# Kernel optimization log

Hardware: AMD Instinct MI355X
Metric: run time of the kernel (lower is better)

The kernel has to match this reference:

```python
import jax, jax.numpy as jnp
import numpy as np

GENETIC_CODE = {'TTT': 'F', 'TTC': 'F', 'TTA': 'L', 'TTG': 'L', 'CTT': 'L', 'CTC': 'L', 'CTA': 'L', 'CTG': 'L', 'ATT': 'I', 'ATC': 'I', 'ATA': 'I', 'ATG': 'M', 'GTT': 'V', 'GTC': 'V', 'GTA': 'V', 'GTG': 'V', 'TCT': 'S', 'TCC': 'S', 'TCA': 'S', 'TCG': 'S', 'AGT': 'S', 'AGC': 'S', 'CCT': 'P', 'CCC': 'P', 'CCA': 'P', 'CCG': 'P', 'ACT': 'T', 'ACC': 'T', 'ACA': 'T', 'ACG': 'T', 'GCT': 'A', 'GCC': 'A', 'GCA': 'A', 'GCG': 'A', 'TAT': 'Y', 'TAC': 'Y', 'TAA': '*', 'TAG': '*', 'TGA': '*', 'CAT': 'H', 'CAC': 'H', 'CAA': 'Q', 'CAG': 'Q', 'AAT': 'N', 'AAC': 'N', 'AAA': 'K', 'AAG': 'K', 'GAT': 'D', 'GAC': 'D', 'GAA': 'E', 'GAG': 'E', 'TGT': 'C', 'TGC': 'C', 'TGG': 'W', 'CGT': 'R', 'CGC': 'R', 'CGA': 'R', 'CGG': 'R', 'AGA': 'R', 'AGG': 'R', 'GGT': 'G', 'GGC': 'G', 'GGA': 'G', 'GGG': 'G'}
NUC_TO_IDX = {'T': 0, 'C': 1, 'A': 2, 'G': 3}

def _build_syn_bias(synonymy_bias=1.0):
    idx = lambda c: NUC_TO_IDX[c[0]] * 16 + NUC_TO_IDX[c[1]] * 4 + NUC_TO_IDX[c[2]]
    groups = {}
    for codon, aa in GENETIC_CODE.items():
        groups.setdefault(aa, []).append(idx(codon))
    m = np.zeros((64, 64), dtype=np.float32)
    for codons in groups.values():
        for i in codons:
            for j in codons:
                m[i, j] = synonymy_bias
    return jnp.asarray(m)

HIDDEN, N_HEADS = 256, 4
HEAD_DIM = HIDDEN // N_HEADS
B, S = 2, 4096

def setup_inputs() -> dict:
    key = jax.random.key(0)
    ks = jax.random.split(key, 10)
    std = 1.0 / np.sqrt(HIDDEN)
    lin = lambda k: jax.random.uniform(k, (HIDDEN, HIDDEN), jnp.float32, -std, std)
    bias = lambda k: jax.random.uniform(k, (HIDDEN,), jnp.float32, -std, std)
    return {
        'x': jax.random.normal(ks[0], (B, S, HIDDEN), jnp.float32),
        'codons': jax.random.randint(ks[1], (B, S), 0, 64),
        'syn_bias': _build_syn_bias(1.0),
        'wq': lin(ks[2]), 'bq': bias(ks[3]),
        'wk': lin(ks[4]), 'bk': bias(ks[5]),
        'wv': lin(ks[6]), 'bv': bias(ks[7]),
        'wo': lin(ks[8]), 'bo': bias(ks[9]),
    }

def reference(x, codons, syn_bias, wq, bq, wk, bk, wv, bv, wo, bo):
    b, s, _ = x.shape
    split = lambda t: t.reshape(b, s, N_HEADS, HEAD_DIM).transpose(0, 2, 1, 3)  # (B,H,S,D)
    q = split(x @ wq.T + bq)
    k = split(x @ wk.T + bk)
    v = split(x @ wv.T + bv)
    scores = jnp.einsum('bhqd,bhkd->bhqk', q, k) / np.sqrt(HEAD_DIM)
    # gather pairwise synonymy bias: (B,S,S) broadcast over heads
    pair_bias = syn_bias[codons[:, :, None], codons[:, None, :]]
    scores = scores + pair_bias[:, None, :, :]
    attn = jax.nn.softmax(scores, axis=-1)
    out = jnp.einsum('bhqk,bhkd->bhqd', attn, v)
    out = out.transpose(0, 2, 1, 3).reshape(b, s, HIDDEN)
    return out @ wo.T + bo
```

## Files before the change

kernel.cpp:

```cpp
#include <hip/hip_runtime.h>
#include <hip/hip_bf16.h>

#define NH 4
#define HD 64
#define HID 256
#define SS 4096

#define QFRAG_PER_HEAD (128 * 6 * 64 * 8)
#define KFRAG_PER_HEAD (64 * 12 * 64 * 8)
#define VFRAG_PER_HEAD (64 * 8 * 64 * 8)

typedef float f4 __attribute__((ext_vector_type(4)));
typedef float f16v __attribute__((ext_vector_type(16)));
typedef short bf8 __attribute__((ext_vector_type(8)));
typedef unsigned int u4v __attribute__((ext_vector_type(4)));

static __device__ __forceinline__ float fast_exp2(float x) {
#if __has_builtin(__builtin_amdgcn_exp2f)
    return __builtin_amdgcn_exp2f(x);
#else
    float r; asm("v_exp_f32 %0, %1" : "=v"(r) : "v"(x)); return r;
#endif
}

static __device__ __forceinline__ unsigned pack2(float a, float b) {
    unsigned ua = (unsigned)__bfloat16_as_ushort(__float2bfloat16(a));
    unsigned ub = (unsigned)__bfloat16_as_ushort(__float2bfloat16(b));
    return ua | (ub << 16);
}

__global__ void setup_kernel(const float* __restrict__ syn,
                             int* __restrict__ gid, float* __restrict__ betaP)
{
    const int lane = threadIdx.x;
    int rep = 64;
    for (int j = 63; j >= 0; --j)
        if (syn[lane * 64 + j] != 0.0f) rep = j;
    if (rep == 64) rep = lane;
    unsigned long long m = __ballot(rep == lane);
    int id = (int)__popcll(m & ((2ull << rep) - 1ull)) - 1;
    if (id < 0) id = 0;
    gid[lane] = id;
    if (lane == 0) *betaP = syn[0] * 1.44269504088896f;
}

__global__ __launch_bounds__(256)
void pack_w_kernel(const float* __restrict__ wq, const float* __restrict__ wk,
                   const float* __restrict__ wv, const float* __restrict__ wo,
                   __hip_bfloat16* __restrict__ wpk)
{
    const int t = blockIdx.x * 256 + threadIdx.x;
    const int mat = t >> 13;
    const int r = t & 8191;
    const int dt = r >> 10, ks = (r >> 6) & 15, lane = r & 63;
    const float* w = (mat == 0) ? wq : (mat == 1) ? wk : (mat == 2) ? wv : wo;
    const int row = dt * 32 + (lane & 31);
    const int col = ks * 16 + (lane >> 5) * 8;
    const f4 a = *(const f4*)&w[(size_t)row * 256 + col];
    const f4 b = *(const f4*)&w[(size_t)row * 256 + col + 4];
    union { unsigned u[4]; bf8 v; } o;
    o.u[0] = pack2(a[0], a[1]); o.u[1] = pack2(a[2], a[3]);
    o.u[2] = pack2(b[0], b[1]); o.u[3] = pack2(b[2], b[3]);
    *(bf8*)&wpk[(size_t)t * 8] = o.v;
}

__global__ __launch_bounds__(256)
void qkv_mfma_kernel(const float* __restrict__ x,
                     const __hip_bfloat16* __restrict__ wpk,
                     const float* __restrict__ bq, const float* __restrict__ bk,
                     const float* __restrict__ bv,
                     const int* __restrict__ codons,
                     const int* __restrict__ gid, const float* __restrict__ betaP,
                     __hip_bfloat16* __restrict__ qfrag,
                     __hip_bfloat16* __restrict__ kfrag,
                     __hip_bfloat16* __restrict__ vfrag)
{
    const int bid = blockIdx.x;
    const int stile = bid / 6;
    const int grp = bid % 6;
    const int tid = threadIdx.x;
    const int w = tid >> 6, lane = tid & 63, hi = lane >> 5, l5 = lane & 31;

    const int bidx = stile >> 7;
    const int stl = stile & 127;
    const int hs = stl & 1, tkv = stl >> 1;

    __shared__ __hip_bfloat16 xs[32][256];

    {
        const int r0 = tid >> 5, c = tid & 31;
        #pragma unroll
        for (int it = 0; it < 4; ++it) {
            const int row = r0 + it * 8;
            const f4 a = *(const f4*)&x[(size_t)(stile * 32 + row) * HID + c * 8];
            const f4 b2 = *(const f4*)&x[(size_t)(stile * 32 + row) * HID + c * 8 + 4];
            union { unsigned u[4]; bf8 v; } o;
            o.u[0] = pack2(a[0], a[1]); o.u[1] = pack2(a[2], a[3]);
            o.u[2] = pack2(b2[0], b2[1]); o.u[3] = pack2(b2[2], b2[3]);
            *(bf8*)&xs[row][((c ^ row) & 31) * 8] = o.v;
        }
    }
    __syncthreads();

    const int t24 = grp * 4 + w;
    const int mat = t24 >> 3;
    const int dt = t24 & 7;
    const int head = dt >> 1, d32 = dt & 1;

    const __hip_bfloat16* wb = wpk + (size_t)((mat * 8 + dt) * 16) * 512 + (size_t)lane * 8;
    bf8 wf[16];
    #pragma unroll
    for (int ks = 0; ks < 16; ++ks) wf[ks] = *(const bf8*)&wb[ks * 512];

    f16v acc;
    #pragma unroll
    for (int r = 0; r < 16; ++r) acc[r] = 0.0f;

    if (mat < 2) {
        #pragma unroll
        for (int ks = 0; ks < 16; ++ks) {
            const bf8 xf = *(const bf8*)&xs[l5][(((ks * 2 + hi) ^ l5) & 31) * 8];
            acc = __builtin_amdgcn_mfma_f32_32x32x16_bf16(wf[ks], xf, acc, 0, 0, 0);
        }
    } else {
        #pragma unroll
        for (int ks = 0; ks < 16; ++ks) {
            const bf8 xf = *(const bf8*)&xs[l5][(((ks * 2 + hi) ^ l5) & 31) * 8];
            acc = __builtin_amdgcn_mfma_f32_32x32x16_bf16(xf, wf[ks], acc, 0, 0, 0);
        }
    }

    const float QSCALE = 0.18033688011112042f;
    if (mat == 0) {
        f4 b4[4];
        #pragma unroll
        for (int j = 0; j < 4; ++j)
            b4[j] = *(const f4*)&bq[head * 64 + d32 * 32 + j * 8 + 4 * hi];
        #pragma unroll
        for (int r = 0; r < 16; ++r) acc[r] = (acc[r] + b4[r >> 2][r & 3]) * QSCALE;
    } else if (mat == 1) {
        f4 b4[4];
        #pragma unroll
        for (int j = 0; j < 4; ++j)
            b4[j] = *(const f4*)&bk[head * 64 + d32 * 32 + j * 8 + 4 * hi];
        #pragma unroll
        for (int r = 0; r < 16; ++r) acc[r] += b4[r >> 2][r & 3];
    } else {
        const float bn = bv[head * 64 + d32 * 32 + l5];
        #pragma unroll
        for (int r = 0; r < 16; ++r) acc[r] += bn;
    }

    unsigned wd[8];
    #pragma unroll
    for (int i = 0; i < 8; ++i) wd[i] = pack2(acc[2 * i], acc[2 * i + 1]);
    const unsigned e0 = (unsigned)__shfl_xor((int)(hi ? wd[0] : wd[2]), 32, 64);
    const unsigned e1 = (unsigned)__shfl_xor((int)(hi ? wd[1] : wd[3]), 32, 64);
    const unsigned e2 = (unsigned)__shfl_xor((int)(hi ? wd[4] : wd[6]), 32, 64);
    const unsigned e3 = (unsigned)__shfl_xor((int)(hi ? wd[5] : wd[7]), 32, 64);
    union { unsigned u[4]; bf8 v; } fa, fb;
    if (hi == 0) {
        fa.u[0] = wd[0]; fa.u[1] = wd[1]; fa.u[2] = e0; fa.u[3] = e1;
        fb.u[0] = wd[4]; fb.u[1] = wd[5]; fb.u[2] = e2; fb.u[3] = e3;
    } else {
        fa.u[0] = e0; fa.u[1] = e1; fa.u[2] = wd[2]; fa.u[3] = wd[3];
        fb.u[0] = e2; fb.u[1] = e3; fb.u[2] = wd[6]; fb.u[3] = wd[7];
    }

    const int hd = bidx * NH + head;
    if (mat == 0) {
        __hip_bfloat16* qb = qfrag + (size_t)hd * QFRAG_PER_HEAD;
        *(bf8*)&qb[((size_t)(stl * 6 + d32 * 2 + 0) * 64 + lane) * 8] = fa.v;
        *(bf8*)&qb[((size_t)(stl * 6 + d32 * 2 + 1) * 64 + lane) * 8] = fb.v;
    } else if (mat == 1) {
        __hip_bfloat16* kb = kfrag + (size_t)hd * KFRAG_PER_HEAD;
        *(bf8*)&kb[((size_t)(tkv * 12 + d32 * 4 + hs) * 64 + lane) * 8] = fa.v;
        *(bf8*)&kb[((size_t)(tkv * 12 + d32 * 4 + 2 + hs) * 64 + lane) * 8] = fb.v;
    } else {
        __hip_bfloat16* vb = vfrag + (size_t)hd * VFRAG_PER_HEAD;
        const int ja = ((stl * 2 + 0) & 3) * 2 + d32;
        const int jb = ((stl * 2 + 1) & 3) * 2 + d32;
        *(bf8*)&vb[((size_t)(tkv * 8 + ja) * 64 + lane) * 8] = fa.v;
        *(bf8*)&vb[((size_t)(tkv * 8 + jb) * 64 + lane) * 8] = fb.v;
    }

    if (grp == 0) {
        const int hh = w;
        const int hd2 = bidx * NH + hh;
        __hip_bfloat16* qb = qfrag + (size_t)hd2 * QFRAG_PER_HEAD;
        __hip_bfloat16* kb = kfrag + (size_t)hd2 * KFRAG_PER_HEAD;
        u4v z; z[0] = 0; z[1] = 0; z[2] = 0; z[3] = 0;
        *(u4v*)&qb[((size_t)(stl * 6 + 4) * 64 + lane) * 8] = z;
        *(u4v*)&qb[((size_t)(stl * 6 + 5) * 64 + lane) * 8] = z;
        *(u4v*)&kb[((size_t)(tkv * 12 + 8 + hs) * 64 + lane) * 8] = z;
        *(u4v*)&kb[((size_t)(tkv * 12 + 10 + hs) * 64 + lane) * 8] = z;
        asm volatile("s_waitcnt vmcnt(0)" ::: "memory");
        if (hi == 0) {
            const int cg = gid[codons[bidx * SS + stl * 32 + l5] & 63];
            const float bl2e = *betaP;
            const int lt = ((cg >> 3) & 1) * 32 + l5;
            qb[((size_t)(stl * 6 + 4 + (cg >> 4)) * 64 + lt) * 8 + (cg & 7)] =
                __float2bfloat16(bl2e);
            kb[((size_t)(tkv * 12 + 8 + (cg >> 4) * 2 + hs) * 64 + lt) * 8 + (cg & 7)] =
                __float2bfloat16(1.0f);
        }
    }
}

__global__ __launch_bounds__(256, 3)
void attn_kernel(const __hip_bfloat16* __restrict__ qfrag,
                 const __hip_bfloat16* __restrict__ kfrag,
                 const __hip_bfloat16* __restrict__ vfrag,
                 __hip_bfloat16* __restrict__ po0,
                 __hip_bfloat16* __restrict__ po1,
                 __hip_bfloat16* __restrict__ po2,
                 __hip_bfloat16* __restrict__ po3,
                 float* __restrict__ ls0, float* __restrict__ ls1,
                 float* __restrict__ ls2, float* __restrict__ ls3)
{
    const int bid = blockIdx.x;
    const int bh = bid & 7;
    const int b = bh >> 2, h = bh & 3;
    const int quarter = (bid >> 3) & 3;
    const int qg = bid >> 5;
    const int tid = threadIdx.x;
    const int w = tid >> 6;
    const int lane = tid & 63;
    const int q5 = lane & 31;
    const int hi = lane >> 5;

    __shared__ __align__(16) char smem[40960];
    __shared__ float l_sh[128];

    const char* kT = (const char*)(kfrag + (size_t)(b * NH + h) * KFRAG_PER_HEAD);
    const char* vT = (const char*)(vfrag + (size_t)(b * NH + h) * VFRAG_PER_HEAD);

    const int stl = qg * 4 + w;
    const __hip_bfloat16* qb = qfrag + (size_t)(b * NH + h) * QFRAG_PER_HEAD
                               + ((size_t)stl * 6 * 64 + lane) * 8;
    bf8 qf[6];
    #pragma unroll
    for (int ks = 0; ks < 6; ++ks) qf[ks] = *(const bf8*)&qb[ks * 512];

    f16v oacc0, oacc1;
    #pragma unroll
    for (int r = 0; r < 16; ++r) { oacc0[r] = 0.0f; oacc1[r] = 0.0f; }
    float lrun = 0.0f;

    const int w5 = w * 5;
    bf8 g[5];

    auto loadG = [&](int tt) {
        #pragma unroll
        for (int c = 0; c < 5; ++c) {
            const int id = w5 + c;
            const char* src = (id < 12)
                ? kT + (size_t)tt * 12288 + (size_t)id * 1024
                : vT + (size_t)tt * 8192 + (size_t)(id - 12) * 1024;
            g[c] = *(const bf8*)(src + lane * 16);
        }
    };
    auto writeL = [&](int buf) {
        #pragma unroll
        for (int c = 0; c < 5; ++c) {
            const int id = w5 + c;
            *(bf8*)&smem[buf * 20480 + id * 1024 + lane * 16] = g[c];
        }
    };

    const int tt0 = quarter * 16;
    loadG(tt0);
    writeL(0);
    __syncthreads();

    int cur = 0;
    #pragma unroll 1
    for (int t = 0; t < 16; ++t) {
        if (t + 1 < 16) loadG(tt0 + t + 1);

        const char* kb = smem + cur * 20480 + lane * 16;

        f16v sA, sB;
        #pragma unroll
        for (int r = 0; r < 16; ++r) { sA[r] = 0.0f; sB[r] = 0.0f; }
        __builtin_amdgcn_s_setprio(1);
        #pragma unroll
        for (int ks = 0; ks < 6; ++ks) {
            const bf8 k0 = *(const bf8*)(kb + (2 * ks) * 1024);
            const bf8 k1 = *(const bf8*)(kb + (2 * ks + 1) * 1024);
            sA = __builtin_amdgcn_mfma_f32_32x32x16_bf16(k0, qf[ks], sA, 0, 0, 0);
            sB = __builtin_amdgcn_mfma_f32_32x32x16_bf16(k1, qf[ks], sB, 0, 0, 0);
        }
        __builtin_amdgcn_s_setprio(0);

        float ls = 0.0f;
        #pragma unroll
        for (int r = 0; r < 16; ++r) { sA[r] = fast_exp2(sA[r]); ls += sA[r]; }
        #pragma unroll
        for (int r = 0; r < 16; ++r) { sB[r] = fast_exp2(sB[r]); ls += sB[r]; }
        lrun += ls;

        unsigned dwv[2][4][2];
        #pragma unroll
        for (int j = 0; j < 4; ++j)
            #pragma unroll
            for (int c = 0; c < 2; ++c) {
                dwv[0][j][c] = pack2(sA[j * 4 + 2 * c], sA[j * 4 + 2 * c + 1]);
                dwv[1][j][c] = pack2(sB[j * 4 + 2 * c], sB[j * 4 + 2 * c + 1]);
            }
        unsigned rc[2][2][2];
        #pragma unroll
        for (int t2 = 0; t2 < 2; ++t2)
            #pragma unroll
            for (int k1 = 0; k1 < 2; ++k1)
                #pragma unroll
                for (int c = 0; c < 2; ++c) {
                    const unsigned snd = hi ? dwv[t2][2 * k1][c] : dwv[t2][2 * k1 + 1][c];
                    rc[t2][k1][c] = (unsigned)__shfl_xor((int)snd, 32, 64);
                }
        bf8 pfv[4];
        #pragma unroll
        for (int ks = 0; ks < 4; ++ks) {
            const int t2 = ks >> 1, k1 = ks & 1;
            union { unsigned u[4]; bf8 v; } pu;
            pu.u[0] = hi ? rc[t2][k1][0] : dwv[t2][2 * k1][0];
            pu.u[1] = hi ? rc[t2][k1][1] : dwv[t2][2 * k1][1];
            pu.u[2] = hi ? dwv[t2][2 * k1 + 1][0] : rc[t2][k1][0];
            pu.u[3] = hi ? dwv[t2][2 * k1 + 1][1] : rc[t2][k1][1];
            pfv[ks] = pu.v;
        }

        __builtin_amdgcn_s_setprio(1);
        #pragma unroll
        for (int ks = 0; ks < 4; ++ks) {
            const bf8 v0 = *(const bf8*)(kb + (12 + 2 * ks) * 1024);
            const bf8 v1 = *(const bf8*)(kb + (13 + 2 * ks) * 1024);
            oacc0 = __builtin_amdgcn_mfma_f32_32x32x16_bf16(v0, pfv[ks], oacc0, 0, 0, 0);
            oacc1 = __builtin_amdgcn_mfma_f32_32x32x16_bf16(v1, pfv[ks], oacc1, 0, 0, 0);
        }
        __builtin_amdgcn_s_setprio(0);

        if (t + 1 < 16) writeL(cur ^ 1);
        __syncthreads();
        cur ^= 1;
    }

    const float ltot = lrun + __shfl_xor(lrun, 32, 64);
    float* osh = (float*)smem;
    #pragma unroll
    for (int r = 0; r < 16; ++r) {
        const int d = (r & 3) + 8 * (r >> 2) + 4 * hi;
        osh[(w * 32 + q5) * 68 + d] = oacc0[r];
        osh[(w * 32 + q5) * 68 + 32 + d] = oacc1[r];
    }
    if (hi == 0) l_sh[w * 32 + q5] = ltot;
    __syncthreads();

    __hip_bfloat16* pob = (quarter == 0) ? po0 : (quarter == 1) ? po1
                        : (quarter == 2) ? po2 : po3;
    float* lsb = (quarter == 0) ? ls0 : (quarter == 1) ? ls1
               : (quarter == 2) ? ls2 : ls3;
    const int row = tid >> 1;
    const int dh = (tid & 1) * 32;
    const float* src = &osh[row * 68 + dh];
    __hip_bfloat16* dst = pob + ((size_t)(b * SS + qg * 128 + row) * HID + h * HD + dh);
    #pragma unroll
    for (int j = 0; j < 4; ++j) {
        const f4 x0 = *(const f4*)&src[j * 8];
        const f4 x1 = *(const f4*)&src[j * 8 + 4];
        union { unsigned u[4]; bf8 v; } o;
        o.u[0] = pack2(x0[0], x0[1]); o.u[1] = pack2(x0[2], x0[3]);
        o.u[2] = pack2(x1[0], x1[1]); o.u[3] = pack2(x1[2], x1[3]);
        *(bf8*)&dst[j * 8] = o.v;
    }
    if (tid < 128) lsb[(size_t)(b * SS + qg * 128 + tid) * 4 + h] = l_sh[tid];
}

__global__ __launch_bounds__(256)
void out_proj_kernel(const __hip_bfloat16* __restrict__ po0,
                     const __hip_bfloat16* __restrict__ po1,
                     const __hip_bfloat16* __restrict__ po2,
                     const __hip_bfloat16* __restrict__ po3,
                     const float* __restrict__ ls0, const float* __restrict__ ls1,
                     const float* __restrict__ ls2, const float* __restrict__ ls3,
                     const __hip_bfloat16* __restrict__ wpk,
                     const float* __restrict__ bo, float* __restrict__ out)
{
    const int bid = blockIdx.x;
    const int stile = bid >> 1, grp = bid & 1;
    const int tid = threadIdx.x;
    const int w = tid >> 6, lane = tid & 63, hi = lane >> 5, l5 = lane & 31;

    __shared__ __hip_bfloat16 xs[32][256];
    {
        const int r0 = tid >> 5, c = tid & 31;
        #pragma unroll
        for (int it = 0; it < 4; ++it) {
            const int row = r0 + it * 8;
            const size_t srow = (size_t)stile * 32 + row;
            const int head = c >> 3;
            const float inv = 1.0f / (ls0[srow * 4 + head] + ls1[srow * 4 + head]
                                    + ls2[srow * 4 + head] + ls3[srow * 4 + head]);
            union { bf8 v; unsigned u[4]; } a0, a1, a2, a3;
            a0.v = *(const bf8*)&po0[srow * 256 + c * 8];
            a1.v = *(const bf8*)&po1[srow * 256 + c * 8];
            a2.v = *(const bf8*)&po2[srow * 256 + c * 8];
            a3.v = *(const bf8*)&po3[srow * 256 + c * 8];
            union { unsigned u[4]; bf8 v; } o;
            #pragma unroll
            for (int i = 0; i < 4; ++i) {
                const float lo = __uint_as_float(a0.u[i] << 16)
                               + __uint_as_float(a1.u[i] << 16)
                               + __uint_as_float(a2.u[i] << 16)
                               + __uint_as_float(a3.u[i] << 16);
                const float hv = __uint_as_float(a0.u[i] & 0xffff0000u)
                               + __uint_as_float(a1.u[i] & 0xffff0000u)
                               + __uint_as_float(a2.u[i] & 0xffff0000u)
                               + __uint_as_float(a3.u[i] & 0xffff0000u);
                o.u[i] = pack2(lo * inv, hv * inv);
            }
            *(bf8*)&xs[row][((c ^ row) & 31) * 8] = o.v;
        }
    }
    __syncthreads();

    const int nt = grp * 4 + w;
    const __hip_bfloat16* wb = wpk + (size_t)((3 * 8 + nt) * 16) * 512 + (size_t)lane * 8;
    bf8 wf[16];
    #pragma unroll
    for (int ks = 0; ks < 16; ++ks) wf[ks] = *(const bf8*)&wb[ks * 512];

    f16v acc;
    #pragma unroll
    for (int r = 0; r < 16; ++r) acc[r] = 0.0f;
    #pragma unroll
    for (int ks = 0; ks < 16; ++ks) {
        const bf8 xf = *(const bf8*)&xs[l5][(((ks * 2 + hi) ^ l5) & 31) * 8];
        acc = __builtin_amdgcn_mfma_f32_32x32x16_bf16(xf, wf[ks], acc, 0, 0, 0);
    }

    const float bn = bo[nt * 32 + l5];
    #pragma unroll
    for (int r = 0; r < 16; ++r) {
        const int sloc = (r & 3) + 8 * (r >> 2) + 4 * hi;
        out[(size_t)(stile * 32 + sloc) * HID + nt * 32 + l5] = acc[r] + bn;
    }
}

extern "C" void kernel_launch(void* const* d_in, const int* in_sizes, int n_in,
                              void* d_out, int out_size, void* d_ws, size_t ws_size,
                              hipStream_t stream)
{
    (void)in_sizes; (void)n_in; (void)out_size; (void)ws_size;
    const float* x        = (const float*)d_in[0];
    const int*   codons   = (const int*)d_in[1];
    const float* syn_bias = (const float*)d_in[2];
    const float* wq = (const float*)d_in[3];
    const float* bq = (const float*)d_in[4];
    const float* wk = (const float*)d_in[5];
    const float* bk = (const float*)d_in[6];
    const float* wv = (const float*)d_in[7];
    const float* bv = (const float*)d_in[8];
    const float* wo = (const float*)d_in[9];
    const float* bo = (const float*)d_in[10];
    float* out = (float*)d_out;

    char* ws = (char*)d_ws;
    int*   gid   = (int*)(ws);
    float* betaP = (float*)(ws + 256);
    __hip_bfloat16* wpk   = (__hip_bfloat16*)(ws + 4096);
    __hip_bfloat16* qfrag = (__hip_bfloat16*)(ws + (size_t)1048576u);
    __hip_bfloat16* kfrag = (__hip_bfloat16*)(ws + (size_t)7340032u);
    __hip_bfloat16* vfrag = (__hip_bfloat16*)(ws + (size_t)13631488u);
    __hip_bfloat16* po0   = (__hip_bfloat16*)(ws + (size_t)17825792u);
    __hip_bfloat16* po1   = (__hip_bfloat16*)(ws + (size_t)22020096u);
    __hip_bfloat16* po2   = (__hip_bfloat16*)(ws + (size_t)26214400u);
    __hip_bfloat16* po3   = (__hip_bfloat16*)(ws + (size_t)30408704u);
    float* ls0            = (float*)(ws + (size_t)34603008u);
    float* ls1            = (float*)(ws + (size_t)34734080u);
    float* ls2            = (float*)(ws + (size_t)34865152u);
    float* ls3            = (float*)(ws + (size_t)34996224u);

    setup_kernel<<<1, 64, 0, stream>>>(syn_bias, gid, betaP);
    pack_w_kernel<<<128, 256, 0, stream>>>(wq, wk, wv, wo, wpk);
    qkv_mfma_kernel<<<1536, 256, 0, stream>>>(x, wpk, bq, bk, bv, codons, gid, betaP,
                                              qfrag, kfrag, vfrag);
    attn_kernel<<<1024, 256, 0, stream>>>(qfrag, kfrag, vfrag,
                                          po0, po1, po2, po3, ls0, ls1, ls2, ls3);
    out_proj_kernel<<<512, 256, 0, stream>>>(po0, po1, po2, po3,
                                             ls0, ls1, ls2, ls3, wpk, bo, out);
}
```

Baseline: 93.42 us.

## Halve attention KV tile and LDS footprint to fit four blocks per CU

Each loop iteration now processes a 32-key half tile instead of a 64-key tile: 32 iterations instead of 16, one score MFMA accumulator instead of two. This halves the double-buffered LDS from 40 KB to 20 KB and raises launch bounds to 4 blocks per CU, so the 1024-block grid may be resident at once. The epilogue stages the output through LDS in two 32-column passes with a padded stride of 33 floats to fit the smaller buffer. The cost is twice as many barriers and less MFMA work per synchronisation. The 16-byte vector reads from the stride-33 rows are not 16-byte aligned, which risks slower or incorrect LDS access.

```diff
diff --git a/kernel.cpp b/kernel.cpp
--- a/kernel.cpp
+++ b/kernel.cpp
@@ -207,7 +207,7 @@
     }
 }
 
-__global__ __launch_bounds__(256, 3)
+__global__ __launch_bounds__(256, 4)
 void attn_kernel(const __hip_bfloat16* __restrict__ qfrag,
                  const __hip_bfloat16* __restrict__ kfrag,
                  const __hip_bfloat16* __restrict__ vfrag,
@@ -229,7 +229,7 @@
     const int q5 = lane & 31;
     const int hi = lane >> 5;
 
-    __shared__ __align__(16) char smem[40960];
+    __shared__ __align__(16) char smem[20480];
     __shared__ float l_sh[128];
 
     const char* kT = (const char*)(kfrag + (size_t)(b * NH + h) * KFRAG_PER_HEAD);
@@ -247,133 +247,136 @@
     for (int r = 0; r < 16; ++r) { oacc0[r] = 0.0f; oacc1[r] = 0.0f; }
     float lrun = 0.0f;
 
-    const int w5 = w * 5;
-    bf8 g[5];
-
-    auto loadG = [&](int tt) {
-        #pragma unroll
-        for (int c = 0; c < 5; ++c) {
-            const int id = w5 + c;
-            const char* src = (id < 12)
-                ? kT + (size_t)tt * 12288 + (size_t)id * 1024
-                : vT + (size_t)tt * 8192 + (size_t)(id - 12) * 1024;
+    const int nck = (w < 2) ? 3 : 2;
+    const int ck0 = (w < 2) ? w * 3 : 6 + (w - 2) * 2;
+    bf8 g[3];
+
+    auto loadG = [&](int u) {
+        const int tkv = quarter * 16 + (u >> 1);
+        const int hs = u & 1;
+        #pragma unroll
+        for (int c = 0; c < 3; ++c) {
+            if (c >= nck) break;
+            const int id = ck0 + c;
+            const char* src = (id < 6)
+                ? kT + (size_t)tkv * 12288 + (size_t)(2 * id + hs) * 1024
+                : vT + (size_t)tkv * 8192 + (size_t)(hs * 4 + (id - 6)) * 1024;
             g[c] = *(const bf8*)(src + lane * 16);
         }
     };
     auto writeL = [&](int buf) {
         #pragma unroll
-        for (int c = 0; c < 5; ++c) {
-            const int id = w5 + c;
-            *(bf8*)&smem[buf * 20480 + id * 1024 + lane * 16] = g[c];
+        for (int c = 0; c < 3; ++c) {
+            if (c >= nck) break;
+            *(bf8*)&smem[buf * 10240 + (ck0 + c) * 1024 + lane * 16] = g[c];
         }
     };
 
-    const int tt0 = quarter * 16;
-    loadG(tt0);
+    loadG(0);
     writeL(0);
     __syncthreads();
 
     int cur = 0;
     #pragma unroll 1
-    for (int t = 0; t < 16; ++t) {
-        if (t + 1 < 16) loadG(tt0 + t + 1);
-
-        const char* kb = smem + cur * 20480 + lane * 16;
-
-        f16v sA, sB;
-        #pragma unroll
-        for (int r = 0; r < 16; ++r) { sA[r] = 0.0f; sB[r] = 0.0f; }
+    for (int u = 0; u < 32; ++u) {
+        if (u + 1 < 32) loadG(u + 1);
+
+        const char* kb = smem + cur * 10240 + lane * 16;
+
+        f16v sacc;
+        #pragma unroll
+        for (int r = 0; r < 16; ++r) sacc[r] = 0.0f;
         __builtin_amdgcn_s_setprio(1);
         #pragma unroll
         for (int ks = 0; ks < 6; ++ks) {
-            const bf8 k0 = *(const bf8*)(kb + (2 * ks) * 1024);
-            const bf8 k1 = *(const bf8*)(kb + (2 * ks + 1) * 1024);
-            sA = __builtin_amdgcn_mfma_f32_32x32x16_bf16(k0, qf[ks], sA, 0, 0, 0);
-            sB = __builtin_amdgcn_mfma_f32_32x32x16_bf16(k1, qf[ks], sB, 0, 0, 0);
+            const bf8 k0 = *(const bf8*)(kb + ks * 1024);
+            sacc = __builtin_amdgcn_mfma_f32_32x32x16_bf16(k0, qf[ks], sacc, 0, 0, 0);
         }
         __builtin_amdgcn_s_setprio(0);
 
         float ls = 0.0f;
         #pragma unroll
-        for (int r = 0; r < 16; ++r) { sA[r] = fast_exp2(sA[r]); ls += sA[r]; }
-        #pragma unroll
-        for (int r = 0; r < 16; ++r) { sB[r] = fast_exp2(sB[r]); ls += sB[r]; }
+        for (int r = 0; r < 16; ++r) { sacc[r] = fast_exp2(sacc[r]); ls += sacc[r]; }
         lrun += ls;
 
-        unsigned dwv[2][4][2];
+        unsigned dwv[4][2];
         #pragma unroll
         for (int j = 0; j < 4; ++j)
             #pragma unroll
+            for (int c = 0; c < 2; ++c)
+                dwv[j][c] = pack2(sacc[j * 4 + 2 * c], sacc[j * 4 + 2 * c + 1]);
+        unsigned rc[2][2];
+        #pragma unroll
+        for (int k1 = 0; k1 < 2; ++k1)
+            #pragma unroll
             for (int c = 0; c < 2; ++c) {
-                dwv[0][j][c] = pack2(sA[j * 4 + 2 * c], sA[j * 4 + 2 * c + 1]);
-                dwv[1][j][c] = pack2(sB[j * 4 + 2 * c], sB[j * 4 + 2 * c + 1]);
+                const unsigned snd = hi ? dwv[2 * k1][c] : dwv[2 * k1 + 1][c];
+                rc[k1][c] = (unsigned)__shfl_xor((int)snd, 32, 64);
             }
-        unsigned rc[2][2][2];
-        #pragma unroll
-        for (int t2 = 0; t2 < 2; ++t2)
-            #pragma unroll
-            for (int k1 = 0; k1 < 2; ++k1)
-                #pragma unroll
-                for (int c = 0; c < 2; ++c) {
-                    const unsigned snd = hi ? dwv[t2][2 * k1][c] : dwv[t2][2 * k1 + 1][c];
-                    rc[t2][k1][c] = (unsigned)__shfl_xor((int)snd, 32, 64);
-                }
-        bf8 pfv[4];
-        #pragma unroll
-        for (int ks = 0; ks < 4; ++ks) {
-            const int t2 = ks >> 1, k1 = ks & 1;
+        bf8 pfv[2];
+        #pragma unroll
+        for (int k1 = 0; k1 < 2; ++k1) {
             union { unsigned u[4]; bf8 v; } pu;
-            pu.u[0] = hi ? rc[t2][k1][0] : dwv[t2][2 * k1][0];
-            pu.u[1] = hi ? rc[t2][k1][1] : dwv[t2][2 * k1][1];
-            pu.u[2] = hi ? dwv[t2][2 * k1 + 1][0] : rc[t2][k1][0];
-            pu.u[3] = hi ? dwv[t2][2 * k1 + 1][1] : rc[t2][k1][1];
-            pfv[ks] = pu.v;
+            pu.u[0] = hi ? rc[k1][0] : dwv[2 * k1][0];
+            pu.u[1] = hi ? rc[k1][1] : dwv[2 * k1][1];
+            pu.u[2] = hi ? dwv[2 * k1 + 1][0] : rc[k1][0];
+            pu.u[3] = hi ? dwv[2 * k1 + 1][1] : rc[k1][1];
+            pfv[k1] = pu.v;
         }
 
         __builtin_amdgcn_s_setprio(1);
         #pragma unroll
-        for (int ks = 0; ks < 4; ++ks) {
-            const bf8 v0 = *(const bf8*)(kb + (12 + 2 * ks) * 1024);
-            const bf8 v1 = *(const bf8*)(kb + (13 + 2 * ks) * 1024);
-            oacc0 = __builtin_amdgcn_mfma_f32_32x32x16_bf16(v0, pfv[ks], oacc0, 0, 0, 0);
-            oacc1 = __builtin_amdgcn_mfma_f32_32x32x16_bf16(v1, pfv[ks], oacc1, 0, 0, 0);
+        for (int k1 = 0; k1 < 2; ++k1) {
+            const bf8 v0 = *(const bf8*)(kb + (6 + 2 * k1) * 1024);
+            const bf8 v1 = *(const bf8*)(kb + (7 + 2 * k1) * 1024);
+            oacc0 = __builtin_amdgcn_mfma_f32_32x32x16_bf16(v0, pfv[k1], oacc0, 0, 0, 0);
+            oacc1 = __builtin_amdgcn_mfma_f32_32x32x16_bf16(v1, pfv[k1], oacc1, 0, 0, 0);
         }
         __builtin_amdgcn_s_setprio(0);
 
-        if (t + 1 < 16) writeL(cur ^ 1);
+        if (u + 1 < 32) writeL(cur ^ 1);
         __syncthreads();
         cur ^= 1;
     }
 
     const float ltot = lrun + __shfl_xor(lrun, 32, 64);
-    float* osh = (float*)smem;
-    #pragma unroll
-    for (int r = 0; r < 16; ++r) {
-        const int d = (r & 3) + 8 * (r >> 2) + 4 * hi;
-        osh[(w * 32 + q5) * 68 + d] = oacc0[r];
-        osh[(w * 32 + q5) * 68 + 32 + d] = oacc1[r];
-    }
-    if (hi == 0) l_sh[w * 32 + q5] = ltot;
-    __syncthreads();
-
     __hip_bfloat16* pob = (quarter == 0) ? po0 : (quarter == 1) ? po1
                         : (quarter == 2) ? po2 : po3;
     float* lsb = (quarter == 0) ? ls0 : (quarter == 1) ? ls1
                : (quarter == 2) ? ls2 : ls3;
-    const int row = tid >> 1;
-    const int dh = (tid & 1) * 32;
-    const float* src = &osh[row * 68 + dh];
-    __hip_bfloat16* dst = pob + ((size_t)(b * SS + qg * 128 + row) * HID + h * HD + dh);
-    #pragma unroll
-    for (int j = 0; j < 4; ++j) {
-        const f4 x0 = *(const f4*)&src[j * 8];
-        const f4 x1 = *(const f4*)&src[j * 8 + 4];
-        union { unsigned u[4]; bf8 v; } o;
-        o.u[0] = pack2(x0[0], x0[1]); o.u[1] = pack2(x0[2], x0[3]);
-        o.u[2] = pack2(x1[0], x1[1]); o.u[3] = pack2(x1[2], x1[3]);
-        *(bf8*)&dst[j * 8] = o.v;
-    }
-    if (tid < 128) lsb[(size_t)(b * SS + qg * 128 + tid) * 4 + h] = l_sh[tid];
+    float* osh = (float*)smem;
+
+    __syncthreads();
+    #pragma unroll
+    for (int pass = 0; pass < 2; ++pass) {
+        #pragma unroll
+        for (int r = 0; r < 16; ++r) {
+            const int d = (r & 3) + 8 * (r >> 2) + 4 * hi;
+            osh[(w * 32 + q5) * 33 + d] = pass ? oacc1[r] : oacc0[r];
+        }
+        if (pass == 0 && hi == 0) l_sh[w * 32 + q5] = ltot;
+        __syncthreads();
+
+        const int row = tid >> 1;
+        const int dh = (tid & 1) * 16;
+        const float* src = &osh[row * 33 + dh];
+        __hip_bfloat16* dst = pob + ((size_t)(b * SS + qg * 128 + row) * HID
+                                     + h * HD + pass * 32 + dh);
+        const f4 x0 = *(const f4*)&src[0];
+        const f4 x1 = *(const f4*)&src[4];
+        const f4 x2 = *(const f4*)&src[8];
+        const f4 x3 = *(const f4*)&src[12];
+        union { unsigned u[4]; bf8 v; } o0, o1;
+        o0.u[0] = pack2(x0[0], x0[1]); o0.u[1] = pack2(x0[2], x0[3]);
+        o0.u[2] = pack2(x1[0], x1[1]); o0.u[3] = pack2(x1[2], x1[3]);
+        o1.u[0] = pack2(x2[0], x2[1]); o1.u[1] = pack2(x2[2], x2[3]);
+        o1.u[2] = pack2(x3[0], x3[1]); o1.u[3] = pack2(x3[2], x3[3]);
+        *(bf8*)&dst[0] = o0.v;
+        *(bf8*)&dst[8] = o1.v;
+        if (pass == 0 && tid < 128)
+            lsb[(size_t)(b * SS + qg * 128 + tid) * 4 + h] = l_sh[tid];
+        __syncthreads();
+    }
 }
 
 __global__ __launch_bounds__(256)
```

Result: no change. 93.19 us (-0.3%).

## Stage K/V tiles with direct global-to-LDS loads and raise attention occupancy

Applied to the files above, without the earlier changes.

The attention kernel's K/V double-buffer staging now uses global_load_lds, which copies global memory straight into shared memory instead of passing it through registers and then storing to LDS. That drops the register staging buffer and the separate LDS write step. With those registers freed, launch bounds go from 3 to 4 blocks per CU. To keep LDS use within the existing 40 KB buffer, the output transpose now uses a row stride of 66 instead of 68, and the separate l_sh array is folded into the same buffer. Score packing uses a single v_cvt_pk_bf16_f32 instruction. Risks: 16-byte LDS reads at the 66-float stride are no longer 16-byte aligned and may bank-conflict. The barrier also has to wait correctly on the asynchronous LDS loads.

```diff
diff --git a/kernel.cpp b/kernel.cpp
--- a/kernel.cpp
+++ b/kernel.cpp
@@ -27,6 +27,12 @@
     unsigned ua = (unsigned)__bfloat16_as_ushort(__float2bfloat16(a));
     unsigned ub = (unsigned)__bfloat16_as_ushort(__float2bfloat16(b));
     return ua | (ub << 16);
+}
+
+static __device__ __forceinline__ unsigned cvtpk(float a, float b) {
+    unsigned r;
+    asm("v_cvt_pk_bf16_f32 %0, %1, %2" : "=v"(r) : "v"(a), "v"(b));
+    return r;
 }
 
 __global__ void setup_kernel(const float* __restrict__ syn,
@@ -207,7 +213,7 @@
     }
 }
 
-__global__ __launch_bounds__(256, 3)
+__global__ __launch_bounds__(256, 4)
 void attn_kernel(const __hip_bfloat16* __restrict__ qfrag,
                  const __hip_bfloat16* __restrict__ kfrag,
                  const __hip_bfloat16* __restrict__ vfrag,
@@ -230,7 +236,6 @@
     const int hi = lane >> 5;
 
     __shared__ __align__(16) char smem[40960];
-    __shared__ float l_sh[128];
 
     const char* kT = (const char*)(kfrag + (size_t)(b * NH + h) * KFRAG_PER_HEAD);
     const char* vT = (const char*)(vfrag + (size_t)(b * NH + h) * VFRAG_PER_HEAD);
@@ -248,35 +253,30 @@
     float lrun = 0.0f;
 
     const int w5 = w * 5;
-    bf8 g[5];
-
-    auto loadG = [&](int tt) {
+    const int tt0 = quarter * 16;
+
+    auto stage = [&](int buf, int t) {
+        const int tt = tt0 + t;
         #pragma unroll
         for (int c = 0; c < 5; ++c) {
             const int id = w5 + c;
             const char* src = (id < 12)
                 ? kT + (size_t)tt * 12288 + (size_t)id * 1024
                 : vT + (size_t)tt * 8192 + (size_t)(id - 12) * 1024;
-            g[c] = *(const bf8*)(src + lane * 16);
+            __builtin_amdgcn_global_load_lds(
+                (const __attribute__((address_space(1))) unsigned int*)(src + lane * 16),
+                (__attribute__((address_space(3))) unsigned int*)(smem + buf * 20480 + id * 1024),
+                16, 0, 0);
         }
     };
-    auto writeL = [&](int buf) {
-        #pragma unroll
-        for (int c = 0; c < 5; ++c) {
-            const int id = w5 + c;
-            *(bf8*)&smem[buf * 20480 + id * 1024 + lane * 16] = g[c];
-        }
-    };
-
-    const int tt0 = quarter * 16;
-    loadG(tt0);
-    writeL(0);
+
+    stage(0, 0);
     __syncthreads();
 
     int cur = 0;
     #pragma unroll 1
     for (int t = 0; t < 16; ++t) {
-        if (t + 1 < 16) loadG(tt0 + t + 1);
+        if (t + 1 < 16) stage(cur ^ 1, t + 1);
 
         const char* kb = smem + cur * 20480 + lane * 16;
 
@@ -305,8 +305,8 @@
         for (int j = 0; j < 4; ++j)
             #pragma unroll
             for (int c = 0; c < 2; ++c) {
-                dwv[0][j][c] = pack2(sA[j * 4 + 2 * c], sA[j * 4 + 2 * c + 1]);
-                dwv[1][j][c] = pack2(sB[j * 4 + 2 * c], sB[j * 4 + 2 * c + 1]);
+                dwv[0][j][c] = cvtpk(sA[j * 4 + 2 * c], sA[j * 4 + 2 * c + 1]);
+                dwv[1][j][c] = cvtpk(sB[j * 4 + 2 * c], sB[j * 4 + 2 * c + 1]);
             }
         unsigned rc[2][2][2];
         #pragma unroll
@@ -340,20 +340,20 @@
         }
         __builtin_amdgcn_s_setprio(0);
 
-        if (t + 1 < 16) writeL(cur ^ 1);
         __syncthreads();
         cur ^= 1;
     }
 
     const float ltot = lrun + __shfl_xor(lrun, 32, 64);
     float* osh = (float*)smem;
+    float* lsh = (float*)(smem + 33792);
     #pragma unroll
     for (int r = 0; r < 16; ++r) {
         const int d = (r & 3) + 8 * (r >> 2) + 4 * hi;
-        osh[(w * 32 + q5) * 68 + d] = oacc0[r];
-        osh[(w * 32 + q5) * 68 + 32 + d] = oacc1[r];
-    }
-    if (hi == 0) l_sh[w * 32 + q5] = ltot;
+        osh[(w * 32 + q5) * 66 + d] = oacc0[r];
+        osh[(w * 32 + q5) * 66 + 32 + d] = oacc1[r];
+    }
+    if (hi == 0) lsh[w * 32 + q5] = ltot;
     __syncthreads();
 
     __hip_bfloat16* pob = (quarter == 0) ? po0 : (quarter == 1) ? po1
@@ -362,7 +362,7 @@
                : (quarter == 2) ? ls2 : ls3;
     const int row = tid >> 1;
     const int dh = (tid & 1) * 32;
-    const float* src = &osh[row * 68 + dh];
+    const float* src = &osh[row * 66 + dh];
     __hip_bfloat16* dst = pob + ((size_t)(b * SS + qg * 128 + row) * HID + h * HD + dh);
     #pragma unroll
     for (int j = 0; j < 4; ++j) {
@@ -373,7 +373,7 @@
         o.u[2] = pack2(x1[0], x1[1]); o.u[3] = pack2(x1[2], x1[3]);
         *(bf8*)&dst[j * 8] = o.v;
     }
-    if (tid < 128) lsb[(size_t)(b * SS + qg * 128 + tid) * 4 + h] = l_sh[tid];
+    if (tid < 128) lsb[(size_t)(b * SS + qg * 128 + tid) * 4 + h] = lsh[tid];
 }
 
 __global__ __launch_bounds__(256)
```

New measurement: 89.77 us. 1.04x faster.
